# Optimization experiments

Measured on AMD Instinct MI355X. Metric: run time of the kernel, lower is better.

Reference implementation:

```python
import jax, jax.numpy as jnp
import numpy as np

D = 512      # bit dimension
M = 131072   # stored reference points
B = 64       # query batch (batchLength in source)
EPS = 1e-6


def setup_inputs() -> dict:
    key = jax.random.key(0)
    k1, k2, k3, k4, k5 = jax.random.split(key, 5)
    return {
        "t_X1_T_bits": jax.random.randint(k1, (D, B), 0, 2, dtype=jnp.int32),
        "t_X2_T_bits": jax.random.randint(k2, (D, M), 0, 2, dtype=jnp.int32),
        # block-packed copy used only by the original custom backward; ignored here
        "t_X2_byDimBlock_T_bits": jax.random.randint(k3, (16, 1024), 0, 2, dtype=jnp.int32),
        "t_Y_knn": jax.random.normal(k4, (M,), dtype=jnp.float32),
        "t_W": jax.random.uniform(k5, (D,), dtype=jnp.float32, minval=0.5, maxval=1.5),
        "alpha": jnp.zeros((), jnp.float32),
        "beta": jnp.ones((), jnp.float32),
        "k": jnp.asarray(0.1, jnp.float32),
        "j": jnp.asarray(0.1, jnp.float32),
    }


def _squash_F(x, k, j):
    # F() from kNNFit: two-stage rational squash
    inner = x * (1 - k) / (k * (1 - 2 * jnp.abs(x)) + 1)
    t = 2 * inner - 1
    return 0.5 + 0.5 * t * (1 + j) / (-j * (1 - 2 * jnp.abs(t)) + 1)


def reference(t_X1_T_bits, t_X2_T_bits, t_X2_byDimBlock_T_bits, t_Y_knn,
              t_W, alpha, beta, k, j):
    # Weighted Hamming distance between every stored point (X2, [D,M]) and
    # every query (X1, [D,B]):
    #   WHD[m,b] = sum_d W[d] * (x1[d,b] XOR x2[d,m])
    # For 0/1 bits: xor = x1 + x2 - 2*x1*x2, so WHD decomposes into two
    # weighted bit-counts plus one GEMM (avoids a [D,M,B] intermediate).
    X1 = t_X1_T_bits.astype(jnp.float32)  # [D,B]
    X2 = t_X2_T_bits.astype(jnp.float32)  # [D,M]
    s1 = t_W @ X1                                            # [B]
    s2 = t_W @ X2                                            # [M]
    cross = jnp.einsum('dm,db->mb', X2, t_W[:, None] * X1)   # [M,B]
    t_WHDx = s1[None, :] + s2[:, None] - 2.0 * cross         # [M,B]

    t_norm_W = jnp.sum(jnp.abs(t_W)) + EPS                   # L1 norm
    t_FQx = _squash_F(1.0 - t_WHDx / t_norm_W, k, j)         # [M,B]
    t_score = jnp.mean(t_FQx * t_Y_knn[:, None], axis=0)     # [B]
    return beta * (t_score + alpha)
```

## Files before the change

kernel.cpp:

```cpp
#include <hip/hip_runtime.h>
#include <hip/hip_bf16.h>


#define DD 512
#define MM 131072
#define BQ 64
#define NWG 1024
#define NWAVES (NWG * 4)
#define WS_BFRAG 0
#define WS_META  65536
#define WS_PART  131072

typedef __attribute__((ext_vector_type(8))) short short8;
typedef __attribute__((ext_vector_type(16))) float floatx16;
typedef __attribute__((ext_vector_type(4))) unsigned int uintx4;

__global__ __launch_bounds__(256) void knn_setup(
    const int* __restrict__ X1, const float* __restrict__ W,
    void* __restrict__ ws) {
  short8* bm = (short8*)((char*)ws + WS_BFRAG);
  float* meta = (float*)((char*)ws + WS_META);
  const int tid = threadIdx.x;
#pragma unroll
  for (int i = 0; i < 16; ++i) {
    const int e = tid + 256 * i;
    const int lane = e & 63, t = (e >> 6) & 1, s = e >> 7;
    const int half = lane >> 5, col = lane & 31;
    const int b = t * 32 + col;
    short8 f;
#pragma unroll
    for (int j = 0; j < 8; ++j) {
      const int d = s * 16 + half * 8 + j;
      unsigned short hb = __builtin_bit_cast(unsigned short, __float2bfloat16(W[d]));
      if (X1[d * BQ + b]) hb ^= 0x8000u;
      f[j] = (short)hb;
    }
    bm[e] = f;
  }
  __shared__ float s1p[4][64];
  const int chunk = tid >> 6, b = tid & 63;
  float s = 0.f;
  for (int d = chunk * 128; d < chunk * 128 + 128; ++d)
    s += W[d] * (float)X1[d * BQ + b];
  s1p[chunk][b] = s;
  __syncthreads();
  if (tid < 64) {
    meta[tid] = s1p[0][tid] + s1p[1][tid] + s1p[2][tid] + s1p[3][tid];
    float nw = 0.f;
#pragma unroll
    for (int j = 0; j < 8; ++j) nw += fabsf(W[tid * 8 + j]);
    nw += __shfl_xor(nw, 32);
    nw += __shfl_xor(nw, 16);
    nw += __shfl_xor(nw, 8);
    nw += __shfl_xor(nw, 4);
    nw += __shfl_xor(nw, 2);
    nw += __shfl_xor(nw, 1);
    if (tid == 0) meta[64] = 1.0f / (nw + 1e-6f);
  }
}

__global__ __launch_bounds__(256, 4) void knn_main(
    const int* __restrict__ X2, const float* __restrict__ Y,
    const float* __restrict__ kp, const float* __restrict__ jp,
    const void* __restrict__ ws_ro, float* __restrict__ partials) {
  const short8* bm = (const short8*)((const char*)ws_ro + WS_BFRAG);
  const float* meta = (const float*)((const char*)ws_ro + WS_META);

  const int tid = threadIdx.x;
  const int wv = tid >> 6, l = tid & 63;
  const int half = l >> 5, col = l & 31;
  const int m0 = blockIdx.x * 128 + wv * 32;

  floatx16 acc0, acc1;
#pragma unroll
  for (int r = 0; r < 16; ++r) { acc0[r] = 0.f; acc1[r] = 0.f; }

  const int* g0 = X2 + (size_t)(half * 8) * MM + m0 + col;
  int v[8], vn[8];
#pragma unroll
  for (int j = 0; j < 8; ++j) v[j] = __builtin_nontemporal_load(g0 + (size_t)j * MM);
  short8 bf0 = bm[0 * 64 + l];
  short8 bf1 = bm[1 * 64 + l];

#pragma unroll
  for (int s = 0; s < 32; ++s) {
    short8 nbf0 = bf0, nbf1 = bf1;
    if (s < 31) {
      const int* g = g0 + (size_t)((s + 1) * 16) * MM;
#pragma unroll
      for (int j = 0; j < 8; ++j) vn[j] = __builtin_nontemporal_load(g + (size_t)j * MM);
      nbf0 = bm[((s + 1) * 2 + 0) * 64 + l];
      nbf1 = bm[((s + 1) * 2 + 1) * 64 + l];
    }
    uintx4 u;
#pragma unroll
    for (int q = 0; q < 4; ++q)
      u[q] = (unsigned int)(v[2 * q] | (v[2 * q + 1] << 16)) * 0x3F80u;
    const short8 af = __builtin_bit_cast(short8, u);
    acc0 = __builtin_amdgcn_mfma_f32_32x32x16_bf16(af, bf0, acc0, 0, 0, 0);
    acc1 = __builtin_amdgcn_mfma_f32_32x32x16_bf16(af, bf1, acc1, 0, 0, 0);
#pragma unroll
    for (int j = 0; j < 8; ++j) v[j] = vn[j];
    bf0 = nbf0; bf1 = nbf1;
  }

  const float inv_norm = meta[64];
  const float kk = kp[0], jj = jp[0];
  const float c1 = 1.0f - kk, c2 = 1.0f + jj;
  const float s1b0 = meta[col];
  const float s1b1 = meta[32 + col];
  float p0 = 0.f, p1 = 0.f;
#pragma unroll
  for (int r = 0; r < 16; ++r) {
    const int ml = (r & 3) + 8 * (r >> 2) + 4 * half;
    const float ym = Y[m0 + ml];
    {
      const float x = 1.0f - (s1b0 + acc0[r]) * inv_norm;
      const float inner = x * c1 / (kk * (1.0f - 2.0f * fabsf(x)) + 1.0f);
      const float t2 = 2.0f * inner - 1.0f;
      const float fq = 0.5f + 0.5f * t2 * c2 / (-jj * (1.0f - 2.0f * fabsf(t2)) + 1.0f);
      p0 += fq * ym;
    }
    {
      const float x = 1.0f - (s1b1 + acc1[r]) * inv_norm;
      const float inner = x * c1 / (kk * (1.0f - 2.0f * fabsf(x)) + 1.0f);
      const float t2 = 2.0f * inner - 1.0f;
      const float fq = 0.5f + 0.5f * t2 * c2 / (-jj * (1.0f - 2.0f * fabsf(t2)) + 1.0f);
      p1 += fq * ym;
    }
  }
  p0 += __shfl_xor(p0, 32);
  p1 += __shfl_xor(p1, 32);
  const int gw = blockIdx.x * 4 + wv;
  if (l < 32) {
    partials[(size_t)col * NWAVES + gw] = p0;
    partials[(size_t)(32 + col) * NWAVES + gw] = p1;
  }
}

__global__ __launch_bounds__(256) void knn_finalize(
    const float* __restrict__ partials, const float* __restrict__ alphap,
    const float* __restrict__ betap, float* __restrict__ out) {
  __shared__ float red[256];
  const int b = blockIdx.x, t = threadIdx.x;
  float s = 0.f;
#pragma unroll
  for (int i = 0; i < NWAVES / 256; ++i)
    s += partials[(size_t)b * NWAVES + i * 256 + t];
  red[t] = s;
  __syncthreads();
  if (t < 64) {
    float x = red[t] + red[t + 64] + red[t + 128] + red[t + 192];
    x += __shfl_xor(x, 32);
    x += __shfl_xor(x, 16);
    x += __shfl_xor(x, 8);
    x += __shfl_xor(x, 4);
    x += __shfl_xor(x, 2);
    x += __shfl_xor(x, 1);
    if (t == 0) out[b] = betap[0] * (x * (1.0f / (float)MM) + alphap[0]);
  }
}

extern "C" void kernel_launch(void* const* d_in, const int* in_sizes, int n_in,
                              void* d_out, int out_size, void* d_ws, size_t ws_size,
                              hipStream_t stream) {
  const int* X1 = (const int*)d_in[0];
  const int* X2 = (const int*)d_in[1];
  const float* Y = (const float*)d_in[3];
  const float* W = (const float*)d_in[4];
  const float* alphap = (const float*)d_in[5];
  const float* betap = (const float*)d_in[6];
  const float* kp = (const float*)d_in[7];
  const float* jp = (const float*)d_in[8];

  float* partials = (float*)((char*)d_ws + WS_PART);

  knn_setup<<<1, 256, 0, stream>>>(X1, W, d_ws);
  knn_main<<<NWG, 256, 0, stream>>>(X2, Y, kp, jp, d_ws, partials);
  knn_finalize<<<BQ, 256, 0, stream>>>(partials, alphap, betap, (float*)d_out);
}
```

Measured before the change: 383.5 us.

## Load X2 with 128-bit vector loads and transpose through per-wave LDS

```diff
diff --git a/kernel.cpp b/kernel.cpp
--- a/kernel.cpp
+++ b/kernel.cpp
@@ -14,6 +14,7 @@
 typedef __attribute__((ext_vector_type(8))) short short8;
 typedef __attribute__((ext_vector_type(16))) float floatx16;
 typedef __attribute__((ext_vector_type(4))) unsigned int uintx4;
+typedef __attribute__((ext_vector_type(4))) int intx4;
 
 __global__ __launch_bounds__(256) void knn_setup(
     const int* __restrict__ X1, const float* __restrict__ W,
@@ -66,41 +67,65 @@
   const short8* bm = (const short8*)((const char*)ws_ro + WS_BFRAG);
   const float* meta = (const float*)((const char*)ws_ro + WS_META);
 
+  __shared__ __align__(16) unsigned int lds[4][2][320];
+
   const int tid = threadIdx.x;
   const int wv = tid >> 6, l = tid & 63;
   const int half = l >> 5, col = l & 31;
   const int m0 = blockIdx.x * 128 + wv * 32;
+  unsigned int (*buf)[320] = lds[wv];
+
+  const int r = l >> 3;
+  const int mo = (l & 7) * 4;
+  const int wbase = mo * 10 + r;
+  const int rbase = col * 10 + half * 4;
 
   floatx16 acc0, acc1;
 #pragma unroll
-  for (int r = 0; r < 16; ++r) { acc0[r] = 0.f; acc1[r] = 0.f; }
-
-  const int* g0 = X2 + (size_t)(half * 8) * MM + m0 + col;
-  int v[8], vn[8];
-#pragma unroll
-  for (int j = 0; j < 8; ++j) v[j] = __builtin_nontemporal_load(g0 + (size_t)j * MM);
+  for (int q = 0; q < 16; ++q) { acc0[q] = 0.f; acc1[q] = 0.f; }
+
+  const int* g0 = X2 + (size_t)(2 * r) * MM + m0 + mo;
+
+  intx4 ca, cb, na, nb;
+  {
+    const int* p = g0;
+    ca = __builtin_nontemporal_load((const intx4*)p);
+    cb = __builtin_nontemporal_load((const intx4*)(p + MM));
+  }
+#pragma unroll
+  for (int i = 0; i < 4; ++i)
+    buf[0][wbase + 10 * i] = (unsigned int)(ca[i] | (cb[i] << 16)) * 0x3F80u;
+  {
+    const int* p = g0 + (size_t)16 * MM;
+    na = __builtin_nontemporal_load((const intx4*)p);
+    nb = __builtin_nontemporal_load((const intx4*)(p + MM));
+  }
   short8 bf0 = bm[0 * 64 + l];
   short8 bf1 = bm[1 * 64 + l];
 
 #pragma unroll
   for (int s = 0; s < 32; ++s) {
+    uint2 lo = *(const uint2*)&buf[s & 1][rbase];
+    uint2 hi = *(const uint2*)&buf[s & 1][rbase + 2];
+    uintx4 u;
+    u[0] = lo.x; u[1] = lo.y; u[2] = hi.x; u[3] = hi.y;
+    const short8 af = __builtin_bit_cast(short8, u);
     short8 nbf0 = bf0, nbf1 = bf1;
     if (s < 31) {
-      const int* g = g0 + (size_t)((s + 1) * 16) * MM;
-#pragma unroll
-      for (int j = 0; j < 8; ++j) vn[j] = __builtin_nontemporal_load(g + (size_t)j * MM);
+#pragma unroll
+      for (int i = 0; i < 4; ++i)
+        buf[(s + 1) & 1][wbase + 10 * i] =
+            (unsigned int)(na[i] | (nb[i] << 16)) * 0x3F80u;
       nbf0 = bm[((s + 1) * 2 + 0) * 64 + l];
       nbf1 = bm[((s + 1) * 2 + 1) * 64 + l];
     }
-    uintx4 u;
-#pragma unroll
-    for (int q = 0; q < 4; ++q)
-      u[q] = (unsigned int)(v[2 * q] | (v[2 * q + 1] << 16)) * 0x3F80u;
-    const short8 af = __builtin_bit_cast(short8, u);
+    if (s < 30) {
+      const int* p = g0 + (size_t)(s + 2) * 16 * MM;
+      na = __builtin_nontemporal_load((const intx4*)p);
+      nb = __builtin_nontemporal_load((const intx4*)(p + MM));
+    }
     acc0 = __builtin_amdgcn_mfma_f32_32x32x16_bf16(af, bf0, acc0, 0, 0, 0);
     acc1 = __builtin_amdgcn_mfma_f32_32x32x16_bf16(af, bf1, acc1, 0, 0, 0);
-#pragma unroll
-    for (int j = 0; j < 8; ++j) v[j] = vn[j];
     bf0 = nbf0; bf1 = nbf1;
   }
 
@@ -111,18 +136,18 @@
   const float s1b1 = meta[32 + col];
   float p0 = 0.f, p1 = 0.f;
 #pragma unroll
-  for (int r = 0; r < 16; ++r) {
-    const int ml = (r & 3) + 8 * (r >> 2) + 4 * half;
+  for (int q = 0; q < 16; ++q) {
+    const int ml = (q & 3) + 8 * (q >> 2) + 4 * half;
     const float ym = Y[m0 + ml];
     {
-      const float x = 1.0f - (s1b0 + acc0[r]) * inv_norm;
+      const float x = 1.0f - (s1b0 + acc0[q]) * inv_norm;
       const float inner = x * c1 / (kk * (1.0f - 2.0f * fabsf(x)) + 1.0f);
       const float t2 = 2.0f * inner - 1.0f;
       const float fq = 0.5f + 0.5f * t2 * c2 / (-jj * (1.0f - 2.0f * fabsf(t2)) + 1.0f);
       p0 += fq * ym;
     }
     {
-      const float x = 1.0f - (s1b1 + acc1[r]) * inv_norm;
+      const float x = 1.0f - (s1b1 + acc1[q]) * inv_norm;
       const float inner = x * c1 / (kk * (1.0f - 2.0f * fabsf(x)) + 1.0f);
       const float t2 = 2.0f * inner - 1.0f;
       const float fq = 0.5f + 0.5f * t2 * c2 / (-jj * (1.0f - 2.0f * fabsf(t2)) + 1.0f);
```

After: 384.1 us. No clear change (+0.2%).
